# Optimization experiments

Measured on AMD Instinct MI355X. Metric: run time of the kernel, lower is better.

Reference implementation:

```python
import jax, jax.numpy as jnp
import numpy as np

B, L, D_MODEL, H, DK, DV = 4, 2048, 1024, 16, 64, 64


def setup_inputs() -> dict:
    key = jax.random.key(0)
    ks = jax.random.split(key, 11)
    s = 1.0 / np.sqrt(D_MODEL)
    return {
        "queries": jax.random.normal(ks[0], (B, L, D_MODEL), jnp.float32),
        "keys": jax.random.normal(ks[1], (B, L, D_MODEL), jnp.float32),
        "values": jax.random.normal(ks[2], (B, L, D_MODEL), jnp.float32),
        "Wq": jax.random.normal(ks[3], (D_MODEL, H * DK), jnp.float32) * s,
        "bq": jnp.zeros((H * DK,), jnp.float32),
        "Wk": jax.random.normal(ks[4], (D_MODEL, H * DK), jnp.float32) * s,
        "bk": jnp.zeros((H * DK,), jnp.float32),
        "Wv": jax.random.normal(ks[5], (D_MODEL, H * DV), jnp.float32) * s,
        "bv": jnp.zeros((H * DV,), jnp.float32),
        "Wo": jax.random.normal(ks[6], (H * DV, D_MODEL), jnp.float32) * s,
        "bo": jnp.zeros((D_MODEL,), jnp.float32),
    }


def reference(queries, keys, values, Wq, bq, Wk, bk, Wv, bv, Wo, bo):
    b, l, _ = queries.shape
    s = keys.shape[1]
    q = (queries @ Wq + bq).reshape(b, l, H, DK)
    k = (keys @ Wk + bk).reshape(b, s, H, DK)
    v = (values @ Wv + bv).reshape(b, s, H, DV)
    scale = 1.0 / np.sqrt(DK)
    scores = jnp.einsum("blhe,bshe->bhls", q, k)  # [B,H,L,S]
    causal = jnp.triu(jnp.ones((l, s), bool), k=1)
    scores = jnp.where(causal[None, None], -jnp.inf, scores)
    A = jax.nn.softmax(scale * scores, axis=-1)
    out = jnp.einsum("bhls,bshd->blhd", A, v).reshape(b, l, H * DV)
    return out @ Wo + bo
```

## Files before the change

### kernel.cpp

```cpp
#include <hip/hip_runtime.h>

typedef __attribute__((ext_vector_type(8))) short s8v;
typedef __attribute__((ext_vector_type(4))) short s4v;
typedef __attribute__((ext_vector_type(4))) float f4v;
typedef __attribute__((ext_vector_type(4))) unsigned int u4v;

#define LOG2E 1.44269504088896340736f

__device__ __forceinline__ unsigned short f2bf(float f) {
    unsigned int x = __float_as_uint(f);
    return (unsigned short)((x + 0x7fffu + ((x >> 16) & 1u)) >> 16);
}
__device__ __forceinline__ s8v ld8(const unsigned short* p) {
    return *(const s8v*)p;
}
__device__ __forceinline__ s8v cvt8(const float* p) {
    f4v lo = *(const f4v*)p, hi = *(const f4v*)(p + 4);
    s8v r;
    r[0] = (short)f2bf(lo[0]); r[1] = (short)f2bf(lo[1]);
    r[2] = (short)f2bf(lo[2]); r[3] = (short)f2bf(lo[3]);
    r[4] = (short)f2bf(hi[0]); r[5] = (short)f2bf(hi[1]);
    r[6] = (short)f2bf(hi[2]); r[7] = (short)f2bf(hi[3]);
    return r;
}

#define GLOAD_LDS(g, l) __builtin_amdgcn_global_load_lds(              \
    (const __attribute__((address_space(1))) void*)(const void*)(g),   \
    (__attribute__((address_space(3))) void*)(void*)(l), 16, 0, 0)

__global__ __launch_bounds__(256) void transpose_w(
    const float* __restrict__ W, unsigned short* __restrict__ Wt)
{
    __shared__ float tile[32][33];
    int tx = threadIdx.x, ty = threadIdx.y;
    int x = blockIdx.x * 32 + tx;
#pragma unroll
    for (int i = 0; i < 4; i++) {
        int y = blockIdx.y * 32 + ty + i * 8;
        tile[ty + i * 8][tx] = W[y * 1024 + x];
    }
    __syncthreads();
    int x2 = blockIdx.y * 32 + tx;
#pragma unroll
    for (int i = 0; i < 4; i++) {
        int y2 = blockIdx.x * 32 + ty + i * 8;
        Wt[y2 * 1024 + x2] = f2bf(tile[tx][ty + i * 8]);
    }
}

__global__ __launch_bounds__(256) void cvt_bf16(
    const float* __restrict__ in, unsigned short* __restrict__ out, int n8)
{
    int stride = gridDim.x * 256;
    for (int i = blockIdx.x * 256 + threadIdx.x; i < n8; i += stride)
        *(s8v*)(out + (size_t)i * 8) = cvt8(in + (size_t)i * 8);
}

__global__ __launch_bounds__(256) void gemm128(
    const unsigned short* __restrict__ A,
    const unsigned short* __restrict__ Bt,
    const float* __restrict__ bias,
    void* __restrict__ outv, int mode, float oscale)
{
    __shared__ __align__(16) unsigned short ldsA[2][128 * 32];
    __shared__ __align__(16) unsigned short ldsB[2][128 * 32];

    int tid = threadIdx.x;
    int w = tid >> 6, lane = tid & 63;
    int quad = lane >> 4, l15 = lane & 15;
    int wr = w >> 1, wc = w & 1;
    int m0 = blockIdx.y * 128, n0 = blockIdx.x * 128;

    int crow = tid >> 2, ck = (tid & 3) * 8;

    f4v acc[4][4];
#pragma unroll
    for (int m = 0; m < 4; m++)
#pragma unroll
        for (int n = 0; n < 4; n++) { f4v z = {0.f, 0.f, 0.f, 0.f}; acc[m][n] = z; }

    auto stage = [&](int buf, int k0) {
        const unsigned short* ga = A + (size_t)(m0 + crow) * 1024 + k0 + ck;
        GLOAD_LDS(ga, &ldsA[buf][w * 512]);
        GLOAD_LDS(ga + (size_t)64 * 1024, &ldsA[buf][2048 + w * 512]);
        const unsigned short* gb = Bt + (size_t)(n0 + crow) * 1024 + k0 + ck;
        GLOAD_LDS(gb, &ldsB[buf][w * 512]);
        GLOAD_LDS(gb + (size_t)64 * 1024, &ldsB[buf][2048 + w * 512]);
    };

    stage(0, 0);
    __syncthreads();
    for (int t = 0; t < 32; t++) {
        int buf = t & 1;
        if (t < 31) stage(buf ^ 1, (t + 1) * 32);
        s8v af[4], bfr[4];
#pragma unroll
        for (int m = 0; m < 4; m++)
            af[m] = *(const s8v*)&ldsA[buf][(wr * 64 + m * 16 + l15) * 32 + quad * 8];
#pragma unroll
        for (int n = 0; n < 4; n++)
            bfr[n] = *(const s8v*)&ldsB[buf][(wc * 64 + n * 16 + l15) * 32 + quad * 8];
#pragma unroll
        for (int m = 0; m < 4; m++)
#pragma unroll
            for (int n = 0; n < 4; n++)
                acc[m][n] = __builtin_amdgcn_mfma_f32_16x16x32_bf16(af[m], bfr[n], acc[m][n], 0, 0, 0);
        __syncthreads();
    }

#pragma unroll
    for (int n = 0; n < 4; n++) {
        int col = n0 + wc * 64 + n * 16 + l15;
        float bvf = bias[col];
#pragma unroll
        for (int m = 0; m < 4; m++) {
#pragma unroll
            for (int r = 0; r < 4; r++) {
                int row = m0 + wr * 64 + m * 16 + quad * 4 + r;
                float v = (acc[m][n][r] + bvf) * oscale;
                if (mode == 0) {
                    ((float*)outv)[(size_t)row * 1024 + col] = v;
                } else {
                    unsigned short* out = (unsigned short*)outv;
                    int bb = row >> 11, l = row & 2047;
                    int hh = col >> 6, d = col & 63;
                    if (mode == 1) {
                        out[(((size_t)bb * 16 + hh) * 2048 + l) * 64 + d] = f2bf(v);
                    } else {
                        int j = l & 63;
                        int s = ((j & 0x0C) << 2) | ((j & 0x02) << 2) |
                                ((j & 0x30) >> 3) | (j & 1);
                        int lp = (l & ~63) | s;
                        out[(((size_t)bb * 16 + hh) * 64 + d) * 2048 + lp] = f2bf(v);
                    }
                }
            }
        }
    }
}

__global__ __launch_bounds__(256) void attn_kernel(
    const unsigned short* __restrict__ Q,
    const unsigned short* __restrict__ K,
    const unsigned short* __restrict__ Vt,
    unsigned short* __restrict__ O)
{
    __shared__ __align__(16) unsigned short Kb[2][64 * 64];
    __shared__ __align__(16) unsigned short Vb[2][64 * 64];

    int tid = threadIdx.x;
    int w = tid >> 6, lane = tid & 63;
    int quad = lane >> 4, l15 = lane & 15;

    int bid = blockIdx.x;
    int swz = (bid & 7) * 128 + (bid >> 3);
    int xp = swz & 15;
    int h = (swz >> 4) & 15;
    int b = swz >> 8;
    int bh = b * 16 + h;

    int srow = tid >> 3;
    int soff = ((tid & 7) * 16) ^ ((srow & 7) << 4);
    const unsigned short* Kbase = K + (size_t)bh * 2048 * 64;
    const unsigned short* Vbase = Vt + (size_t)bh * 64 * 2048;

    auto stageK = [&](int buf, int kt) {
        const unsigned short* g1 = Kbase + (size_t)(kt * 64 + srow) * 64 + (soff >> 1);
        GLOAD_LDS(g1, &Kb[buf][w * 512]);
        GLOAD_LDS(g1 + (size_t)32 * 64, &Kb[buf][2048 + w * 512]);
    };
    auto stageV = [&](int buf, int kt) {
        const unsigned short* g1 = Vbase + (size_t)srow * 2048 + kt * 64 + (soff >> 1);
        GLOAD_LDS(g1, &Vb[buf][w * 512]);
        GLOAD_LDS(g1 + (size_t)32 * 2048, &Vb[buf][2048 + w * 512]);
    };

    int rswz = (l15 & 7) << 4;

#pragma unroll 1
    for (int half = 0; half < 2; half++) {
        int qt = half ? 31 - xp : xp;
        int m0 = qt * 64 + w * 16;

        const unsigned short* qb = Q + ((size_t)bh * 2048 + m0 + l15) * 64 + quad * 8;
        s8v aq0 = ld8(qb), aq1 = ld8(qb + 32);

        float mrun = -1e30f, lsum = 0.f;
        f4v oacc[4];
#pragma unroll
        for (int t = 0; t < 4; t++) { f4v z = {0.f, 0.f, 0.f, 0.f}; oacc[t] = z; }

        stageK(0, 0);
        stageV(0, 0);
        __syncthreads();

#pragma unroll 1
        for (int kt = 0; kt <= qt; kt++) {
            int buf = kt & 1;
            if (kt < qt) { stageK(buf ^ 1, kt + 1); stageV(buf ^ 1, kt + 1); }

            f4v sacc[4];
#pragma unroll
            for (int t = 0; t < 4; t++) { f4v z = {0.f, 0.f, 0.f, 0.f}; sacc[t] = z; }
            const char* kbp = (const char*)&Kb[buf][0];
#pragma unroll
            for (int t = 0; t < 4; t++) {
                int rb = (t * 16 + l15) * 128;
                s8v k0 = *(const s8v*)(kbp + rb + ((quad * 16) ^ rswz));
                s8v k1 = *(const s8v*)(kbp + rb + ((64 + quad * 16) ^ rswz));
                sacc[t] = __builtin_amdgcn_mfma_f32_16x16x32_bf16(k0, aq0, sacc[t], 0, 0, 0);
                sacc[t] = __builtin_amdgcn_mfma_f32_16x16x32_bf16(k1, aq1, sacc[t], 0, 0, 0);
            }

            if (kt == qt) {
                int qrow = w * 16 + l15;
#pragma unroll
                for (int t = 0; t < 4; t++)
#pragma unroll
                    for (int r = 0; r < 4; r++) {
                        int key = t * 16 + quad * 4 + r;
                        if (key > qrow) sacc[t][r] = -1e30f;
                    }
            }

            float mx = sacc[0][0];
#pragma unroll
            for (int t = 0; t < 4; t++)
#pragma unroll
                for (int r = 0; r < 4; r++)
                    mx = fmaxf(mx, sacc[t][r]);
            mx = fmaxf(mx, __shfl_xor(mx, 16));
            mx = fmaxf(mx, __shfl_xor(mx, 32));

            if (__any(mx > mrun + 8.0f)) {
                float mnew = fmaxf(mrun, mx);
                float alpha = exp2f(mrun - mnew);
                lsum *= alpha;
#pragma unroll
                for (int r = 0; r < 4; r++) {
                    float ar = __shfl(alpha, quad * 4 + r);
#pragma unroll
                    for (int t2 = 0; t2 < 4; t2++) oacc[t2][r] *= ar;
                }
                mrun = mnew;
            }

            float rs = 0.f;
#pragma unroll
            for (int t = 0; t < 4; t++)
#pragma unroll
                for (int r = 0; r < 4; r++) {
                    float p = exp2f(sacc[t][r] - mrun);
                    rs += p;
                    sacc[t][r] = p;
                }
            lsum += rs;

            unsigned int pwv[4][2];
#pragma unroll
            for (int t = 0; t < 4; t++) {
                asm("v_cvt_pk_bf16_f32 %0, %1, %2"
                    : "=v"(pwv[t][0]) : "v"(sacc[t][0]), "v"(sacc[t][1]));
                asm("v_cvt_pk_bf16_f32 %0, %1, %2"
                    : "=v"(pwv[t][1]) : "v"(sacc[t][2]), "v"(sacc[t][3]));
            }

            const char* vbp = (const char*)&Vb[buf][0];
#pragma unroll
            for (int c = 0; c < 2; c++) {
                u4v aw;
                aw[0] = pwv[0][c]; aw[1] = pwv[1][c];
                aw[2] = pwv[2][c]; aw[3] = pwv[3][c];
                s8v apf = __builtin_bit_cast(s8v, aw);
#pragma unroll
                for (int t2 = 0; t2 < 4; t2++) {
                    int rb = (t2 * 16 + l15) * 128;
                    s8v bvv = *(const s8v*)(vbp + rb + ((quad * 32 + c * 16) ^ rswz));
                    oacc[t2] = __builtin_amdgcn_mfma_f32_16x16x32_bf16(apf, bvv, oacc[t2], 0, 0, 0);
                }
            }
            __syncthreads();
        }

        float ltot = lsum;
        ltot += __shfl_xor(ltot, 16);
        ltot += __shfl_xor(ltot, 32);
        float inv = 1.f / ltot;
#pragma unroll
        for (int r = 0; r < 4; r++) {
            float ir = __shfl(inv, quad * 4 + r);
            int l = m0 + quad * 4 + r;
#pragma unroll
            for (int t2 = 0; t2 < 4; t2++) {
                O[((size_t)b * 2048 + l) * 1024 + h * 64 + t2 * 16 + l15] = f2bf(oacc[t2][r] * ir);
            }
        }
    }
}

extern "C" void kernel_launch(void* const* d_in, const int* in_sizes, int n_in,
                              void* d_out, int out_size, void* d_ws, size_t ws_size,
                              hipStream_t stream)
{
    const float* queries = (const float*)d_in[0];
    const float* keys    = (const float*)d_in[1];
    const float* values  = (const float*)d_in[2];
    const float* Wq = (const float*)d_in[3];
    const float* bq = (const float*)d_in[4];
    const float* Wk = (const float*)d_in[5];
    const float* bk = (const float*)d_in[6];
    const float* Wv = (const float*)d_in[7];
    const float* bv = (const float*)d_in[8];
    const float* Wo = (const float*)d_in[9];
    const float* bo = (const float*)d_in[10];

    unsigned short* ws = (unsigned short*)d_ws;
    const size_t M1 = 1u << 20, M8 = 8u << 20;
    unsigned short* WqT = ws;
    unsigned short* WkT = ws + 1 * M1;
    unsigned short* WvT = ws + 2 * M1;
    unsigned short* WoT = ws + 3 * M1;
    unsigned short* qw  = ws + 4 * M1;
    unsigned short* kw  = qw + M8;
    unsigned short* vtw = kw + M8;
    unsigned short* ow  = vtw + M8;

    const float sscale = 0.125f * LOG2E;

    dim3 tb(32, 8), tg(32, 32);
    transpose_w<<<tg, tb, 0, stream>>>(Wq, WqT);
    transpose_w<<<tg, tb, 0, stream>>>(Wk, WkT);
    transpose_w<<<tg, tb, 0, stream>>>(Wv, WvT);
    transpose_w<<<tg, tb, 0, stream>>>(Wo, WoT);

    dim3 gg(8, 64);
    const int n8 = (int)(M8 / 8);
    cvt_bf16<<<2048, 256, 0, stream>>>(queries, ow, n8);
    gemm128<<<gg, 256, 0, stream>>>(ow, WqT, bq, qw, 1, sscale);
    cvt_bf16<<<2048, 256, 0, stream>>>(keys, ow, n8);
    gemm128<<<gg, 256, 0, stream>>>(ow, WkT, bk, kw, 1, 1.0f);
    cvt_bf16<<<2048, 256, 0, stream>>>(values, ow, n8);
    gemm128<<<gg, 256, 0, stream>>>(ow, WvT, bv, vtw, 2, 1.0f);

    attn_kernel<<<dim3(1024), 256, 0, stream>>>(qw, kw, vtw, ow);

    gemm128<<<gg, 256, 0, stream>>>(ow, WoT, bo, d_out, 0, 1.0f);
}
```

Measured before the change: 413.0 us.

## Fuse fp32-to-bf16 conversion into batched QKV GEMM and merge weight transposes

Removes the three standalone fp32-to-bf16 conversion kernels. The QKV projection GEMM now loads fp32 activations directly, converts them in registers with packed bf16 conversion instructions, and writes them to LDS. Q, K and V projections run as one 1536-block launch with a chiplet-aware block remap, and the four weight transposes are merged into one launch. This cuts a full write and re-read of the bf16 activation buffers plus several launches, at the cost of register-staged A loads instead of direct global-to-LDS copies.

```diff
diff --git a/kernel.cpp b/kernel.cpp
--- a/kernel.cpp
+++ b/kernel.cpp
@@ -14,24 +14,21 @@
 __device__ __forceinline__ s8v ld8(const unsigned short* p) {
     return *(const s8v*)p;
 }
-__device__ __forceinline__ s8v cvt8(const float* p) {
-    f4v lo = *(const f4v*)p, hi = *(const f4v*)(p + 4);
-    s8v r;
-    r[0] = (short)f2bf(lo[0]); r[1] = (short)f2bf(lo[1]);
-    r[2] = (short)f2bf(lo[2]); r[3] = (short)f2bf(lo[3]);
-    r[4] = (short)f2bf(hi[0]); r[5] = (short)f2bf(hi[1]);
-    r[6] = (short)f2bf(hi[2]); r[7] = (short)f2bf(hi[3]);
-    return r;
-}
 
 #define GLOAD_LDS(g, l) __builtin_amdgcn_global_load_lds(              \
     (const __attribute__((address_space(1))) void*)(const void*)(g),   \
     (__attribute__((address_space(3))) void*)(void*)(l), 16, 0, 0)
 
-__global__ __launch_bounds__(256) void transpose_w(
-    const float* __restrict__ W, unsigned short* __restrict__ Wt)
+__global__ __launch_bounds__(256) void transpose_w4(
+    const float* __restrict__ W0, const float* __restrict__ W1,
+    const float* __restrict__ W2, const float* __restrict__ W3,
+    unsigned short* __restrict__ T0, unsigned short* __restrict__ T1,
+    unsigned short* __restrict__ T2, unsigned short* __restrict__ T3)
 {
     __shared__ float tile[32][33];
+    int z = blockIdx.z;
+    const float* W = z == 0 ? W0 : z == 1 ? W1 : z == 2 ? W2 : W3;
+    unsigned short* Wt = z == 0 ? T0 : z == 1 ? T1 : z == 2 ? T2 : T3;
     int tx = threadIdx.x, ty = threadIdx.y;
     int x = blockIdx.x * 32 + tx;
 #pragma unroll
@@ -48,36 +45,156 @@
     }
 }
 
-__global__ __launch_bounds__(256) void cvt_bf16(
-    const float* __restrict__ in, unsigned short* __restrict__ out, int n8)
-{
-    int stride = gridDim.x * 256;
-    for (int i = blockIdx.x * 256 + threadIdx.x; i < n8; i += stride)
-        *(s8v*)(out + (size_t)i * 8) = cvt8(in + (size_t)i * 8);
-}
-
-__global__ __launch_bounds__(256) void gemm128(
-    const unsigned short* __restrict__ A,
-    const unsigned short* __restrict__ Bt,
-    const float* __restrict__ bias,
-    void* __restrict__ outv, int mode, float oscale)
+__global__ __launch_bounds__(256) void qkv_gemm(
+    const float* __restrict__ Aq, const float* __restrict__ Ak,
+    const float* __restrict__ Avv,
+    const unsigned short* __restrict__ BtQ, const unsigned short* __restrict__ BtK,
+    const unsigned short* __restrict__ BtV,
+    const float* __restrict__ bq, const float* __restrict__ bk,
+    const float* __restrict__ bv,
+    unsigned short* __restrict__ qo, unsigned short* __restrict__ ko,
+    unsigned short* __restrict__ vo, float sscale)
 {
     __shared__ __align__(16) unsigned short ldsA[2][128 * 32];
     __shared__ __align__(16) unsigned short ldsB[2][128 * 32];
+
+    int i = blockIdx.x;
+    int c = i & 7, j = i >> 3;
+    int bx = j & 7, zy = c * 24 + (j >> 3);
+    int z = zy >> 6, by = zy & 63;
+
+    const float* A = z == 0 ? Aq : z == 1 ? Ak : Avv;
+    const unsigned short* Bt = z == 0 ? BtQ : z == 1 ? BtK : BtV;
+    const float* bias = z == 0 ? bq : z == 1 ? bk : bv;
+    unsigned short* out = z == 0 ? qo : z == 1 ? ko : vo;
+    float oscale = z == 0 ? sscale : 1.0f;
 
     int tid = threadIdx.x;
     int w = tid >> 6, lane = tid & 63;
     int quad = lane >> 4, l15 = lane & 15;
     int wr = w >> 1, wc = w & 1;
-    int m0 = blockIdx.y * 128, n0 = blockIdx.x * 128;
-
+    int m0 = by * 128, n0 = bx * 128;
+
+    int arow = tid >> 1, ahs = tid & 1;
     int crow = tid >> 2, ck = (tid & 3) * 8;
 
+    const float* ap = A + (size_t)(m0 + arow) * 1024 + ahs * 16;
+    const unsigned short* bp = Bt + (size_t)(n0 + crow) * 1024 + ck;
+    unsigned short* aw0 = &ldsA[0][arow * 32 + ahs * 16];
+    unsigned short* aw1 = &ldsA[1][arow * 32 + ahs * 16];
+
     f4v acc[4][4];
 #pragma unroll
     for (int m = 0; m < 4; m++)
 #pragma unroll
-        for (int n = 0; n < 4; n++) { f4v z = {0.f, 0.f, 0.f, 0.f}; acc[m][n] = z; }
+        for (int n = 0; n < 4; n++) { f4v zz = {0.f, 0.f, 0.f, 0.f}; acc[m][n] = zz; }
+
+    auto stageB = [&](int buf, int k0) {
+        GLOAD_LDS(bp + k0, &ldsB[buf][w * 512]);
+        GLOAD_LDS(bp + k0 + (size_t)64 * 1024, &ldsB[buf][2048 + w * 512]);
+    };
+    auto cvtwrA = [&](unsigned short* dst, f4v a0, f4v a1, f4v a2, f4v a3) {
+        unsigned int w0, w1, w2, w3, w4, w5, w6, w7;
+        asm("v_cvt_pk_bf16_f32 %0, %1, %2" : "=v"(w0) : "v"(a0[0]), "v"(a0[1]));
+        asm("v_cvt_pk_bf16_f32 %0, %1, %2" : "=v"(w1) : "v"(a0[2]), "v"(a0[3]));
+        asm("v_cvt_pk_bf16_f32 %0, %1, %2" : "=v"(w2) : "v"(a1[0]), "v"(a1[1]));
+        asm("v_cvt_pk_bf16_f32 %0, %1, %2" : "=v"(w3) : "v"(a1[2]), "v"(a1[3]));
+        asm("v_cvt_pk_bf16_f32 %0, %1, %2" : "=v"(w4) : "v"(a2[0]), "v"(a2[1]));
+        asm("v_cvt_pk_bf16_f32 %0, %1, %2" : "=v"(w5) : "v"(a2[2]), "v"(a2[3]));
+        asm("v_cvt_pk_bf16_f32 %0, %1, %2" : "=v"(w6) : "v"(a3[0]), "v"(a3[1]));
+        asm("v_cvt_pk_bf16_f32 %0, %1, %2" : "=v"(w7) : "v"(a3[2]), "v"(a3[3]));
+        u4v lo; lo[0] = w0; lo[1] = w1; lo[2] = w2; lo[3] = w3;
+        u4v hi; hi[0] = w4; hi[1] = w5; hi[2] = w6; hi[3] = w7;
+        *(u4v*)dst = lo;
+        *(u4v*)(dst + 8) = hi;
+    };
+
+    {
+        f4v a0 = *(const f4v*)(ap), a1 = *(const f4v*)(ap + 4);
+        f4v a2 = *(const f4v*)(ap + 8), a3 = *(const f4v*)(ap + 12);
+        stageB(0, 0);
+        cvtwrA(aw0, a0, a1, a2, a3);
+    }
+    __syncthreads();
+
+    for (int t = 0; t < 32; t++) {
+        int buf = t & 1;
+        bool pf = t < 31;
+        f4v a0, a1, a2, a3;
+        if (pf) {
+            const float* an = ap + (t + 1) * 32;
+            a0 = *(const f4v*)(an); a1 = *(const f4v*)(an + 4);
+            a2 = *(const f4v*)(an + 8); a3 = *(const f4v*)(an + 12);
+            stageB(buf ^ 1, (t + 1) * 32);
+        }
+        s8v af[4], bfr[4];
+#pragma unroll
+        for (int m = 0; m < 4; m++)
+            af[m] = *(const s8v*)&ldsA[buf][(wr * 64 + m * 16 + l15) * 32 + quad * 8];
+#pragma unroll
+        for (int n = 0; n < 4; n++)
+            bfr[n] = *(const s8v*)&ldsB[buf][(wc * 64 + n * 16 + l15) * 32 + quad * 8];
+#pragma unroll
+        for (int m = 0; m < 4; m++)
+#pragma unroll
+            for (int n = 0; n < 4; n++)
+                acc[m][n] = __builtin_amdgcn_mfma_f32_16x16x32_bf16(af[m], bfr[n], acc[m][n], 0, 0, 0);
+        if (pf) cvtwrA(buf ? aw0 : aw1, a0, a1, a2, a3);
+        __syncthreads();
+    }
+
+#pragma unroll
+    for (int n = 0; n < 4; n++) {
+        int col = n0 + wc * 64 + n * 16 + l15;
+        float bvf = bias[col];
+#pragma unroll
+        for (int m = 0; m < 4; m++) {
+#pragma unroll
+            for (int r = 0; r < 4; r++) {
+                int row = m0 + wr * 64 + m * 16 + quad * 4 + r;
+                float v = (acc[m][n][r] + bvf) * oscale;
+                int bb = row >> 11, l = row & 2047;
+                int hh = col >> 6, d = col & 63;
+                if (z != 2) {
+                    out[(((size_t)bb * 16 + hh) * 2048 + l) * 64 + d] = f2bf(v);
+                } else {
+                    int jj = l & 63;
+                    int s = ((jj & 0x0C) << 2) | ((jj & 0x02) << 2) |
+                            ((jj & 0x30) >> 3) | (jj & 1);
+                    int lp = (l & ~63) | s;
+                    out[(((size_t)bb * 16 + hh) * 64 + d) * 2048 + lp] = f2bf(v);
+                }
+            }
+        }
+    }
+}
+
+__global__ __launch_bounds__(256) void ogemm(
+    const unsigned short* __restrict__ A,
+    const unsigned short* __restrict__ Bt,
+    const float* __restrict__ bias,
+    float* __restrict__ out)
+{
+    __shared__ __align__(16) unsigned short ldsA[2][128 * 32];
+    __shared__ __align__(16) unsigned short ldsB[2][128 * 32];
+
+    int i = blockIdx.x;
+    int c = i & 7, j = i >> 3;
+    int bx = j & 7, by = c * 8 + (j >> 3);
+
+    int tid = threadIdx.x;
+    int w = tid >> 6, lane = tid & 63;
+    int quad = lane >> 4, l15 = lane & 15;
+    int wr = w >> 1, wc = w & 1;
+    int m0 = by * 128, n0 = bx * 128;
+
+    int crow = tid >> 2, ck = (tid & 3) * 8;
+
+    f4v acc[4][4];
+#pragma unroll
+    for (int m = 0; m < 4; m++)
+#pragma unroll
+        for (int n = 0; n < 4; n++) { f4v zz = {0.f, 0.f, 0.f, 0.f}; acc[m][n] = zz; }
 
     auto stage = [&](int buf, int k0) {
         const unsigned short* ga = A + (size_t)(m0 + crow) * 1024 + k0 + ck;
@@ -113,29 +230,12 @@
         int col = n0 + wc * 64 + n * 16 + l15;
         float bvf = bias[col];
 #pragma unroll
-        for (int m = 0; m < 4; m++) {
+        for (int m = 0; m < 4; m++)
 #pragma unroll
             for (int r = 0; r < 4; r++) {
                 int row = m0 + wr * 64 + m * 16 + quad * 4 + r;
-                float v = (acc[m][n][r] + bvf) * oscale;
-                if (mode == 0) {
-                    ((float*)outv)[(size_t)row * 1024 + col] = v;
-                } else {
-                    unsigned short* out = (unsigned short*)outv;
-                    int bb = row >> 11, l = row & 2047;
-                    int hh = col >> 6, d = col & 63;
-                    if (mode == 1) {
-                        out[(((size_t)bb * 16 + hh) * 2048 + l) * 64 + d] = f2bf(v);
-                    } else {
-                        int j = l & 63;
-                        int s = ((j & 0x0C) << 2) | ((j & 0x02) << 2) |
-                                ((j & 0x30) >> 3) | (j & 1);
-                        int lp = (l & ~63) | s;
-                        out[(((size_t)bb * 16 + hh) * 64 + d) * 2048 + lp] = f2bf(v);
-                    }
-                }
-            }
-        }
+                out[(size_t)row * 1024 + col] = acc[m][n][r] + bvf;
+            }
     }
 }
 
@@ -327,22 +427,15 @@
 
     const float sscale = 0.125f * LOG2E;
 
-    dim3 tb(32, 8), tg(32, 32);
-    transpose_w<<<tg, tb, 0, stream>>>(Wq, WqT);
-    transpose_w<<<tg, tb, 0, stream>>>(Wk, WkT);
-    transpose_w<<<tg, tb, 0, stream>>>(Wv, WvT);
-    transpose_w<<<tg, tb, 0, stream>>>(Wo, WoT);
-
-    dim3 gg(8, 64);
-    const int n8 = (int)(M8 / 8);
-    cvt_bf16<<<2048, 256, 0, stream>>>(queries, ow, n8);
-    gemm128<<<gg, 256, 0, stream>>>(ow, WqT, bq, qw, 1, sscale);
-    cvt_bf16<<<2048, 256, 0, stream>>>(keys, ow, n8);
-    gemm128<<<gg, 256, 0, stream>>>(ow, WkT, bk, kw, 1, 1.0f);
-    cvt_bf16<<<2048, 256, 0, stream>>>(values, ow, n8);
-    gemm128<<<gg, 256, 0, stream>>>(ow, WvT, bv, vtw, 2, 1.0f);
+    dim3 tb(32, 8);
+    transpose_w4<<<dim3(32, 32, 4), tb, 0, stream>>>(
+        Wq, Wk, Wv, Wo, WqT, WkT, WvT, WoT);
+
+    qkv_gemm<<<dim3(1536), 256, 0, stream>>>(
+        queries, keys, values, WqT, WkT, WvT, bq, bk, bv,
+        qw, kw, vtw, sscale);
 
     attn_kernel<<<dim3(1024), 256, 0, stream>>>(qw, kw, vtw, ow);
 
-    gemm128<<<gg, 256, 0, stream>>>(ow, WoT, bo, d_out, 0, 1.0f);
-}
+    ogemm<<<dim3(512), 256, 0, stream>>>(ow, WoT, bo, (float*)d_out);
+}
```

Measured after the change: 391.7 us. 5.2% less time.

## Triple-buffer GEMM with swizzled LDS, XCD-aware block mapping, and fused weight transposes

Applied to the files above, without the earlier changes.

Rewrites the projection GEMM to use a three-stage LDS ring with explicit vmcnt waits and raw barriers, so that two tiles of global loads are in flight while MFMAs run. It XOR-swizzles the 16-byte k-chunks in LDS to reduce bank conflicts on fragment reads, and remaps a 1D grid so blocks sharing an A row-panel land on the same XCD for L2 reuse. It also raises wave priority around the MFMA block and merges the four weight-transpose launches into one. The cost is more LDS per block (48KB), which may lower occupancy, plus manual waitcnt logic that depends on the exact number of loads issued per stage.

```diff
diff --git a/kernel.cpp b/kernel.cpp
--- a/kernel.cpp
+++ b/kernel.cpp
@@ -28,10 +28,16 @@
     (const __attribute__((address_space(1))) void*)(const void*)(g),   \
     (__attribute__((address_space(3))) void*)(void*)(l), 16, 0, 0)
 
-__global__ __launch_bounds__(256) void transpose_w(
-    const float* __restrict__ W, unsigned short* __restrict__ Wt)
+__global__ __launch_bounds__(256) void transpose_w4(
+    const float* __restrict__ W0, const float* __restrict__ W1,
+    const float* __restrict__ W2, const float* __restrict__ W3,
+    unsigned short* __restrict__ T0, unsigned short* __restrict__ T1,
+    unsigned short* __restrict__ T2, unsigned short* __restrict__ T3)
 {
     __shared__ float tile[32][33];
+    int z = blockIdx.z;
+    const float* W = z == 0 ? W0 : z == 1 ? W1 : z == 2 ? W2 : W3;
+    unsigned short* Wt = z == 0 ? T0 : z == 1 ? T1 : z == 2 ? T2 : T3;
     int tx = threadIdx.x, ty = threadIdx.y;
     int x = blockIdx.x * 32 + tx;
 #pragma unroll
@@ -56,62 +62,88 @@
         *(s8v*)(out + (size_t)i * 8) = cvt8(in + (size_t)i * 8);
 }
 
-__global__ __launch_bounds__(256) void gemm128(
+__global__ __launch_bounds__(256) void gemm_ctd(
     const unsigned short* __restrict__ A,
     const unsigned short* __restrict__ Bt,
     const float* __restrict__ bias,
     void* __restrict__ outv, int mode, float oscale)
 {
-    __shared__ __align__(16) unsigned short ldsA[2][128 * 32];
-    __shared__ __align__(16) unsigned short ldsB[2][128 * 32];
+    __shared__ __align__(16) unsigned short ldsA[3][128 * 32];
+    __shared__ __align__(16) unsigned short ldsB[3][128 * 32];
+
+    int i = blockIdx.x;
+    int c = i & 7, j = i >> 3;
+    int bx = j & 7, by = c * 8 + (j >> 3);
 
     int tid = threadIdx.x;
     int w = tid >> 6, lane = tid & 63;
     int quad = lane >> 4, l15 = lane & 15;
     int wr = w >> 1, wc = w & 1;
-    int m0 = blockIdx.y * 128, n0 = blockIdx.x * 128;
-
-    int crow = tid >> 2, ck = (tid & 3) * 8;
+    int m0 = by * 128, n0 = bx * 128;
+
+    int r1 = tid >> 2, qp = tid & 3;
+    int qs = (qp ^ (r1 & 3)) * 8;
+    const unsigned short* ga1 = A  + (size_t)(m0 + r1) * 1024 + qs;
+    const unsigned short* ga2 = A  + (size_t)(m0 + r1 + 64) * 1024 + qs;
+    const unsigned short* gb1 = Bt + (size_t)(n0 + r1) * 1024 + qs;
+    const unsigned short* gb2 = Bt + (size_t)(n0 + r1 + 64) * 1024 + qs;
 
     f4v acc[4][4];
 #pragma unroll
     for (int m = 0; m < 4; m++)
 #pragma unroll
-        for (int n = 0; n < 4; n++) { f4v z = {0.f, 0.f, 0.f, 0.f}; acc[m][n] = z; }
+        for (int n = 0; n < 4; n++) { f4v zz = {0.f, 0.f, 0.f, 0.f}; acc[m][n] = zz; }
 
     auto stage = [&](int buf, int k0) {
-        const unsigned short* ga = A + (size_t)(m0 + crow) * 1024 + k0 + ck;
-        GLOAD_LDS(ga, &ldsA[buf][w * 512]);
-        GLOAD_LDS(ga + (size_t)64 * 1024, &ldsA[buf][2048 + w * 512]);
-        const unsigned short* gb = Bt + (size_t)(n0 + crow) * 1024 + k0 + ck;
-        GLOAD_LDS(gb, &ldsB[buf][w * 512]);
-        GLOAD_LDS(gb + (size_t)64 * 1024, &ldsB[buf][2048 + w * 512]);
+        GLOAD_LDS(ga1 + k0, &ldsA[buf][w * 512]);
+        GLOAD_LDS(ga2 + k0, &ldsA[buf][2048 + w * 512]);
+        GLOAD_LDS(gb1 + k0, &ldsB[buf][w * 512]);
+        GLOAD_LDS(gb2 + k0, &ldsB[buf][2048 + w * 512]);
     };
 
+    int xr = (l15 & 3) << 4;
+
     stage(0, 0);
-    __syncthreads();
+    stage(1, 32);
+    asm volatile("s_waitcnt vmcnt(4)" ::: "memory");
+    asm volatile("s_barrier" ::: "memory");
+
+    int buf = 0;
     for (int t = 0; t < 32; t++) {
-        int buf = t & 1;
-        if (t < 31) stage(buf ^ 1, (t + 1) * 32);
+        if (t < 30) {
+            int nb = buf + 2; if (nb >= 3) nb -= 3;
+            stage(nb, (t + 2) * 32);
+        }
+        const char* ab = (const char*)&ldsA[buf][0];
+        const char* bb = (const char*)&ldsB[buf][0];
         s8v af[4], bfr[4];
 #pragma unroll
         for (int m = 0; m < 4; m++)
-            af[m] = *(const s8v*)&ldsA[buf][(wr * 64 + m * 16 + l15) * 32 + quad * 8];
+            af[m] = *(const s8v*)(ab + (wr * 64 + m * 16 + l15) * 64 + ((quad * 16) ^ xr));
 #pragma unroll
         for (int n = 0; n < 4; n++)
-            bfr[n] = *(const s8v*)&ldsB[buf][(wc * 64 + n * 16 + l15) * 32 + quad * 8];
+            bfr[n] = *(const s8v*)(bb + (wc * 64 + n * 16 + l15) * 64 + ((quad * 16) ^ xr));
+        __builtin_amdgcn_s_setprio(1);
 #pragma unroll
         for (int m = 0; m < 4; m++)
 #pragma unroll
             for (int n = 0; n < 4; n++)
                 acc[m][n] = __builtin_amdgcn_mfma_f32_16x16x32_bf16(af[m], bfr[n], acc[m][n], 0, 0, 0);
-        __syncthreads();
+        __builtin_amdgcn_s_setprio(0);
+        if (t < 31) {
+            if (t < 30) asm volatile("s_waitcnt vmcnt(4)" ::: "memory");
+            else        asm volatile("s_waitcnt vmcnt(0)" ::: "memory");
+            asm volatile("s_barrier" ::: "memory");
+            __builtin_amdgcn_sched_barrier(0);
+        }
+        buf++; if (buf >= 3) buf = 0;
     }
 
 #pragma unroll
     for (int n = 0; n < 4; n++) {
         int col = n0 + wc * 64 + n * 16 + l15;
         float bvf = bias[col];
+        int hh = col >> 6, d = col & 63;
 #pragma unroll
         for (int m = 0; m < 4; m++) {
 #pragma unroll
@@ -122,16 +154,15 @@
                     ((float*)outv)[(size_t)row * 1024 + col] = v;
                 } else {
                     unsigned short* out = (unsigned short*)outv;
-                    int bb = row >> 11, l = row & 2047;
-                    int hh = col >> 6, d = col & 63;
+                    int bb2 = row >> 11, l = row & 2047;
                     if (mode == 1) {
-                        out[(((size_t)bb * 16 + hh) * 2048 + l) * 64 + d] = f2bf(v);
+                        out[(((size_t)bb2 * 16 + hh) * 2048 + l) * 64 + d] = f2bf(v);
                     } else {
-                        int j = l & 63;
-                        int s = ((j & 0x0C) << 2) | ((j & 0x02) << 2) |
-                                ((j & 0x30) >> 3) | (j & 1);
+                        int jj = l & 63;
+                        int s = ((jj & 0x0C) << 2) | ((jj & 0x02) << 2) |
+                                ((jj & 0x30) >> 3) | (jj & 1);
                         int lp = (l & ~63) | s;
-                        out[(((size_t)bb * 16 + hh) * 64 + d) * 2048 + lp] = f2bf(v);
+                        out[(((size_t)bb2 * 16 + hh) * 64 + d) * 2048 + lp] = f2bf(v);
                     }
                 }
             }
@@ -326,23 +357,20 @@
     unsigned short* ow  = vtw + M8;
 
     const float sscale = 0.125f * LOG2E;
-
-    dim3 tb(32, 8), tg(32, 32);
-    transpose_w<<<tg, tb, 0, stream>>>(Wq, WqT);
-    transpose_w<<<tg, tb, 0, stream>>>(Wk, WkT);
-    transpose_w<<<tg, tb, 0, stream>>>(Wv, WvT);
-    transpose_w<<<tg, tb, 0, stream>>>(Wo, WoT);
-
-    dim3 gg(8, 64);
     const int n8 = (int)(M8 / 8);
+
+    dim3 tb(32, 8);
+    transpose_w4<<<dim3(32, 32, 4), tb, 0, stream>>>(
+        Wq, Wk, Wv, Wo, WqT, WkT, WvT, WoT);
+
     cvt_bf16<<<2048, 256, 0, stream>>>(queries, ow, n8);
-    gemm128<<<gg, 256, 0, stream>>>(ow, WqT, bq, qw, 1, sscale);
+    gemm_ctd<<<512, 256, 0, stream>>>(ow, WqT, bq, qw, 1, sscale);
     cvt_bf16<<<2048, 256, 0, stream>>>(keys, ow, n8);
-    gemm128<<<gg, 256, 0, stream>>>(ow, WkT, bk, kw, 1, 1.0f);
+    gemm_ctd<<<512, 256, 0, stream>>>(ow, WkT, bk, kw, 1, 1.0f);
     cvt_bf16<<<2048, 256, 0, stream>>>(values, ow, n8);
-    gemm128<<<gg, 256, 0, stream>>>(ow, WvT, bv, vtw, 2, 1.0f);
+    gemm_ctd<<<512, 256, 0, stream>>>(ow, WvT, bv, vtw, 2, 1.0f);
 
     attn_kernel<<<dim3(1024), 256, 0, stream>>>(qw, kw, vtw, ow);
 
-    gemm128<<<gg, 256, 0, stream>>>(ow, WoT, bo, d_out, 0, 1.0f);
-}
+    gemm_ctd<<<512, 256, 0, stream>>>(ow, WoT, bo, d_out, 0, 1.0f);
+}
```

Measured after the change: 388.6 us. 5.9% less time.
